# Kernel optimization log

Measured on AMD Instinct MI355X. Metric: run time of the kernel, lower is better.

The kernel has to match this reference:

```python
import jax, jax.numpy as jnp
import numpy as np

# Static dims (from init_kwargs / input_specs)
B, D, H, W, T, C = 1, 16, 32, 32, 4, 128
G, NH = 4, 8
HD = C // NH
NW = (D // G) * (H // G) * (W // G)   # windows per sample
N = G ** 3 * T                         # tokens per window (T-major ordering)
MLP_H = 4 * C
SCALE = 1.0 / float(np.sqrt(HD))
EPS = 1e-5


def _ln(x, g, b):
    m = x.mean(-1, keepdims=True)
    v = ((x - m) ** 2).mean(-1, keepdims=True)
    return (x - m) / jnp.sqrt(v + EPS) * g + b


def setup_inputs() -> dict:
    key = jax.random.key(0)
    ks = jax.random.split(key, 10)
    s = 0.02
    return {
        "x": jax.random.normal(ks[0], (B, D, H, W, T, C), jnp.float32),
        "norm1_g": jnp.ones((C,), jnp.float32),
        "norm1_b": jnp.zeros((C,), jnp.float32),
        "pos_embed": jax.random.normal(ks[1], (G, G, G, C), jnp.float32) * s,
        "time_embed": jax.random.normal(ks[2], (T, 1, 1, 1, C), jnp.float32) * s,
        "qkv_w": jax.random.normal(ks[3], (3 * C, C), jnp.float32) * s,
        "qkv_b": jnp.zeros((3 * C,), jnp.float32),
        "proj_w": jax.random.normal(ks[4], (C, C), jnp.float32) * s,
        "proj_b": jnp.zeros((C,), jnp.float32),
        "conv_w": jax.random.normal(ks[5], (C, 1, 3, 3, 3), jnp.float32) * s,  # depthwise
        "conv_b": jnp.zeros((C,), jnp.float32),
        "exln_g": jnp.ones((C,), jnp.float32),
        "exln_b": jnp.zeros((C,), jnp.float32),
        "norm2_g": jnp.ones((C,), jnp.float32),
        "norm2_b": jnp.zeros((C,), jnp.float32),
        "fc1_w": jax.random.normal(ks[6], (MLP_H, C), jnp.float32) * s,
        "fc1_b": jnp.zeros((MLP_H,), jnp.float32),
        "fc2_w": jax.random.normal(ks[7], (C, MLP_H), jnp.float32) * s,
        "fc2_b": jnp.zeros((C,), jnp.float32),
    }


def reference(x, norm1_g, norm1_b, pos_embed, time_embed, qkv_w, qkv_b,
              proj_w, proj_b, conv_w, conv_b, exln_g, exln_b,
              norm2_g, norm2_b, fc1_w, fc1_b, fc2_w, fc2_b):
    # --- window partition (lsda_flag=0, local SDA; dims divisible by G -> padding=0) ---
    xw = x.reshape(B, D // G, G, H // G, G, W // G, G, T, C)
    xw = xw.transpose(0, 1, 3, 5, 7, 2, 4, 6, 8)   # (B, Dg, Hg, Wg, T, G, G, G, C)
    xw = xw.reshape(B * NW, N, C)                   # token dim is T-major over (T,G,G,G)

    # --- pre-norm + window attention ---
    h = _ln(xw, norm1_g, norm1_b)
    h = h.reshape(B * NW, T, G, G, G, C)
    h = (h + pos_embed + time_embed).reshape(B * NW, N, C)  # learned spatial + temporal PE
    qkv = (h @ qkv_w.T + qkv_b).reshape(B * NW, N, 3, NH, HD).transpose(2, 0, 3, 1, 4)
    q, k, v = qkv[0] * SCALE, qkv[1], qkv[2]        # (B_, NH, N, HD)
    attn = jax.nn.softmax(jnp.einsum('bhnd,bhmd->bhnm', q, k), axis=-1)
    o = jnp.einsum('bhnm,bhmd->bhnd', attn, v).transpose(0, 2, 1, 3).reshape(B * NW, N, C)
    o = o @ proj_w.T + proj_b

    # --- window merge (inverse of partition) ---
    y = o.reshape(B, D // G, H // G, W // G, T, G, G, G, C)
    y = y.transpose(0, 1, 5, 2, 6, 3, 7, 4, 8).reshape(B, D, H, W, T, C)

    # --- depthwise 3x3x3 Conv3d over (D,H,W), T folded into batch, then LN ---
    xc = y.transpose(0, 4, 5, 1, 2, 3).reshape(B * T, C, D, H, W)
    xc = jax.lax.conv_general_dilated(
        xc, conv_w, window_strides=(1, 1, 1),
        padding=((1, 1), (1, 1), (1, 1)),
        feature_group_count=C,
        dimension_numbers=('NCDHW', 'OIDHW', 'NCDHW'))
    xc = xc + conv_b[None, :, None, None, None]
    y = xc.reshape(B, T, C, D, H, W).transpose(0, 3, 4, 5, 1, 2)
    y = _ln(y, exln_g, exln_b)

    # --- MLP with residual: x = mlp(norm2(x)) + x ---
    h2 = _ln(y, norm2_g, norm2_b)
    h2 = jax.nn.gelu(h2 @ fc1_w.T + fc1_b, approximate=False)
    h2 = h2 @ fc2_w.T + fc2_b
    return h2 + y
```

## Files before the change

kernel.cpp:

```cpp
#include <hip/hip_runtime.h>
#include <hip/hip_bf16.h>


typedef __attribute__((ext_vector_type(8))) short  s16x8;
typedef __attribute__((ext_vector_type(4))) short  s16x4;
typedef __attribute__((ext_vector_type(4))) float  f32x4;
typedef __attribute__((ext_vector_type(8))) _Float16 f16x8;
typedef __attribute__((ext_vector_type(4))) _Float16 f16x4;

#define CC    128
#define NWIN  256
#define TOKS  65536
#define SCALE 0.25f
#define LNEPS 1e-5f
#define PD 18
#define PH 34
#define PW 34
#define PSITES (PD*PH*PW)
#define Y1P_SHORTS ((size_t)PSITES*512)

__device__ __forceinline__ float b2f(short s) {
  union { unsigned u; float f; } c; c.u = ((unsigned)(unsigned short)s) << 16; return c.f;
}
__device__ __forceinline__ short f2b(float f) {
  __hip_bfloat16 h = __float2bfloat16(f);
  return *reinterpret_cast<short*>(&h);
}
__device__ __forceinline__ float fast_gelu(float x) {
  float u = 1.595769122f * x * fmaf(0.044715f, x*x, 1.0f);
  return x / (1.0f + __expf(-u));
}

__device__ __forceinline__ f32x4 mfma16x16x16_bf16(s16x4 a, s16x4 b, f32x4 c) {
#if __has_builtin(__builtin_amdgcn_mfma_f32_16x16x16_bf16)
  return __builtin_amdgcn_mfma_f32_16x16x16_bf16(a, b, c, 0, 0, 0);
#elif __has_builtin(__builtin_amdgcn_mfma_f32_16x16x16bf16_1k)
  return __builtin_amdgcn_mfma_f32_16x16x16bf16_1k(a, b, c, 0, 0, 0);
#else
  f32x4 d;
  asm("v_mfma_f32_16x16x16_bf16 %0, %1, %2, %3" : "=v"(d) : "v"(a), "v"(b), "v"(c));
  return d;
#endif
}

__device__ __forceinline__ void gload16(const short* g, short* l) {
  __builtin_amdgcn_global_load_lds(
      (const __attribute__((address_space(1))) void*)g,
      (__attribute__((address_space(3))) void*)l, 16, 0, 0);
}

__global__ void prep_kernel(const float* __restrict__ qkv_w, const float* __restrict__ proj_w,
                            const float* __restrict__ fc1_w, const float* __restrict__ fc2_w,
                            const float* __restrict__ conv_w,
                            __hip_bfloat16* wq, __hip_bfloat16* wp,
                            __hip_bfloat16* w1, __hip_bfloat16* w2, float* cwT) {
  int idx = blockIdx.x * 256 + threadIdx.x;
  if (idx < 49152) {
    wq[idx] = __float2bfloat16(qkv_w[idx]);
  } else if (idx < 65536) {
    wp[idx - 49152] = __float2bfloat16(proj_w[idx - 49152]);
  } else if (idx < 131072) {
    w1[idx - 65536] = __float2bfloat16(fc1_w[idx - 65536]);
  } else if (idx < 196608) {
    w2[idx - 131072] = __float2bfloat16(fc2_w[idx - 131072]);
  } else if (idx < 196608 + 27*128) {
    int j = idx - 196608;
    int tap = j >> 7, c = j & 127;
    cwT[tap*128 + c] = conv_w[c*27 + tap];
  }
}

__global__ __launch_bounds__(256) void border_zero_kernel(short* __restrict__ y1p) {
  int idx = blockIdx.x*256 + threadIdx.x;
  if (idx >= PSITES*64) return;
  int site = idx >> 6;
  int w = site % PW, hh = (site / PW) % PH, d = site / (PW*PH);
  if (d != 0 && d != PD-1 && hh != 0 && hh != PH-1 && w != 0 && w != PW-1) return;
  *(s16x8*)&y1p[(size_t)site*512 + (idx & 63)*8] = (s16x8)0;
}

__global__ __launch_bounds__(256) void ln1_pe_kernel(
    const float* __restrict__ x, const float* __restrict__ g, const float* __restrict__ b,
    const float* __restrict__ pos, const float* __restrict__ te,
    __hip_bfloat16* __restrict__ hb) {
  const int tid = threadIdx.x;
  const int tk = blockIdx.x*8 + (tid >> 5);
  const int c4 = (tid & 31) * 4;
  const int wid = tk >> 8, n = tk & 255;
  const int t = n >> 6, gd = (n >> 4) & 3, gh = (n >> 2) & 3, gw = n & 3;
  const int wd = wid >> 6, wh = (wid >> 3) & 7, ww = wid & 7;
  const int d = wd*4 + gd, h = wh*4 + gh, w = ww*4 + gw;
  const size_t xoff = ((size_t)((d*32 + h)*32 + w)*4 + t) * CC;
  f32x4 v = *(const f32x4*)&x[xoff + c4];
  float s  = (v.x + v.y) + (v.z + v.w);
  float sq = (v.x*v.x + v.y*v.y) + (v.z*v.z + v.w*v.w);
#pragma unroll
  for (int m = 1; m <= 16; m <<= 1) { s += __shfl_xor(s, m); sq += __shfl_xor(sq, m); }
  const float mean = s * (1.f/128.f);
  const float var  = sq * (1.f/128.f) - mean*mean;
  const float rstd = rsqrtf(var + LNEPS);
  const int pb = ((gd*4 + gh)*4 + gw) * CC, tb = t * CC;
  f32x4 gv = *(const f32x4*)&g[c4];
  f32x4 bv = *(const f32x4*)&b[c4];
  f32x4 pv = *(const f32x4*)&pos[pb + c4];
  f32x4 tv = *(const f32x4*)&te[tb + c4];
  s16x4 o;
  o[0] = f2b((v.x - mean)*rstd*gv.x + bv.x + pv.x + tv.x);
  o[1] = f2b((v.y - mean)*rstd*gv.y + bv.y + pv.y + tv.y);
  o[2] = f2b((v.z - mean)*rstd*gv.z + bv.z + pv.z + tv.z);
  o[3] = f2b((v.w - mean)*rstd*gv.w + bv.w + pv.w + tv.w);
  *(s16x4*)&((short*)hb)[(size_t)tk*CC + c4] = o;
}

template <int MODE, int KK>
__global__ __launch_bounds__(256) void gemm_kernel(
    const short* __restrict__ Ag, const short* __restrict__ Wg,
    const float* __restrict__ bias,
    void* __restrict__ out0, const _Float16* __restrict__ resid) {
  __shared__ __align__(16) short As[128*64];
  __shared__ __align__(16) short Bs[128*64];
  const int tid = threadIdx.x;
  const int m0 = blockIdx.x * 128;
  const int n0 = blockIdx.y * 128;
  const int lane = tid & 63, wv = tid >> 6;
  const int wr = wv >> 1, wc = wv & 1;
  const int fr = lane & 15, kg = lane >> 4;

  f32x4 acc[4][4];
#pragma unroll
  for (int i = 0; i < 4; ++i)
#pragma unroll
    for (int j = 0; j < 4; ++j) acc[i][j] = (f32x4)0.f;

#pragma unroll
  for (int kc = 0; kc < KK; kc += 64) {
    __syncthreads();
#pragma unroll
    for (int i = 0; i < 4; ++i) {
      const int e = i*2048 + tid*8;
      const int row = e >> 6, col = e & 63;
      gload16(Ag + (size_t)(m0 + row)*KK + kc + col, &As[i*2048 + wv*512]);
      gload16(Wg + (size_t)(n0 + row)*KK + kc + col, &Bs[i*2048 + wv*512]);
    }
    __syncthreads();
#pragma unroll
    for (int ks = 0; ks < 2; ++ks) {
      s16x8 a[4], b[4];
#pragma unroll
      for (int i = 0; i < 4; ++i)
        a[i] = *(const s16x8*)&As[(wr*64 + i*16 + fr)*64 + ks*32 + kg*8];
#pragma unroll
      for (int j = 0; j < 4; ++j)
        b[j] = *(const s16x8*)&Bs[(wc*64 + j*16 + fr)*64 + ks*32 + kg*8];
#pragma unroll
      for (int i = 0; i < 4; ++i)
#pragma unroll
        for (int j = 0; j < 4; ++j)
          acc[i][j] = __builtin_amdgcn_mfma_f32_16x16x32_bf16(b[j], a[i], acc[i][j], 0, 0, 0);
    }
  }

  const int nbb = n0 + wc*64 + kg*4;
  f32x4 bj4[4];
#pragma unroll
  for (int j = 0; j < 4; ++j) bj4[j] = *(const f32x4*)&bias[nbb + j*16];

#pragma unroll
  for (int i = 0; i < 4; ++i) {
    const int m = m0 + wr*64 + i*16 + fr;
    if constexpr (MODE == 0) {
      short* qs = (short*)out0;
      const int sec = n0 >> 7;
      const float scl = (sec == 0) ? SCALE : 1.0f;
      const int wid = m >> 8, ntok = m & 255;
      const int rowbase = sec*8388608 + (wid*8)*4096 + ntok*16 + (nbb & 15);
#pragma unroll
      for (int j = 0; j < 4; ++j) {
        const int head = ((nbb + j*16) >> 4) & 7;
        f32x4 v = acc[i][j];
        s16x4 o;
        o[0] = f2b(fmaf(v[0], scl, bj4[j].x*scl));
        o[1] = f2b(fmaf(v[1], scl, bj4[j].y*scl));
        o[2] = f2b(fmaf(v[2], scl, bj4[j].z*scl));
        o[3] = f2b(fmaf(v[3], scl, bj4[j].w*scl));
        *(s16x4*)&qs[rowbase + head*4096] = o;
      }
    } else if constexpr (MODE == 1) {
      short* y1o = (short*)out0;
      const int wid = m >> 8, ntok = m & 255;
      const int t = ntok >> 6, gd = (ntok >> 4) & 3, gh = (ntok >> 2) & 3, gw = ntok & 3;
      const int wd = wid >> 6, wh = (wid >> 3) & 7, ww = wid & 7;
      const int sr = (((wd*4 + gd + 1)*PH + wh*4 + gh + 1)*PW + ww*4 + gw + 1)*4 + t;
      const int base = sr*CC + nbb;
#pragma unroll
      for (int j = 0; j < 4; ++j) {
        f32x4 v = acc[i][j];
        s16x4 o;
        o[0] = f2b(v[0] + bj4[j].x); o[1] = f2b(v[1] + bj4[j].y);
        o[2] = f2b(v[2] + bj4[j].z); o[3] = f2b(v[3] + bj4[j].w);
        *(s16x4*)&y1o[base + j*16] = o;
      }
    } else if constexpr (MODE == 2) {
      short* gp = (short*)out0;
      const int base = m*512 + nbb;
#pragma unroll
      for (int j = 0; j < 4; ++j) {
        f32x4 v = acc[i][j];
        s16x4 o;
        o[0] = f2b(fast_gelu(v[0] + bj4[j].x)); o[1] = f2b(fast_gelu(v[1] + bj4[j].y));
        o[2] = f2b(fast_gelu(v[2] + bj4[j].z)); o[3] = f2b(fast_gelu(v[3] + bj4[j].w));
        *(s16x4*)&gp[base + j*16] = o;
      }
    } else {
      float* outp = (float*)out0;
      const int base = m*CC + nbb;
#pragma unroll
      for (int j = 0; j < 4; ++j) {
        f32x4 v = acc[i][j];
        f16x4 rz = *(const f16x4*)&resid[base + j*16];
        f32x4 o;
        o.x = v[0] + bj4[j].x + (float)rz[0]; o.y = v[1] + bj4[j].y + (float)rz[1];
        o.z = v[2] + bj4[j].z + (float)rz[2]; o.w = v[3] + bj4[j].w + (float)rz[3];
        *(f32x4*)&outp[base + j*16] = o;
      }
    }
  }
}

#define KPAD 20
#define VPAD 264
__global__ __launch_bounds__(256) void attn_mfma_kernel(
    const __hip_bfloat16* __restrict__ qb, const __hip_bfloat16* __restrict__ kb,
    const __hip_bfloat16* __restrict__ vb, __hip_bfloat16* __restrict__ ob) {
  __shared__ __align__(16) short kL[256*KPAD];
  __shared__ __align__(16) short vT[16*VPAD];
  const int bh = blockIdx.x;
  const int wid = bh >> 3, head = bh & 7;
  const int tid = threadIdx.x;
  const short* kg = (const short*)kb + (size_t)bh*4096;
  const short* vg = (const short*)vb + (size_t)bh*4096;
  const short* qg = (const short*)qb + (size_t)bh*4096;
  {
    s16x8 a0 = *(const s16x8*)&kg[tid*16];
    s16x8 a1 = *(const s16x8*)&kg[tid*16 + 8];
    *(s16x8*)&kL[tid*KPAD]     = a0;
    *(s16x8*)&kL[tid*KPAD + 8] = a1;
    s16x8 b0 = *(const s16x8*)&vg[tid*16];
    s16x8 b1 = *(const s16x8*)&vg[tid*16 + 8];
#pragma unroll
    for (int d = 0; d < 8; ++d) {
      vT[d*VPAD + tid]     = b0[d];
      vT[(d+8)*VPAD + tid] = b1[d];
    }
  }
  __syncthreads();
  const int wv = tid >> 6, lane = tid & 63;
  const int fr = lane & 15, hi = lane >> 4;
  s16x4 kfrag[16], vfrag[16];
#pragma unroll
  for (int t = 0; t < 16; ++t) {
    kfrag[t] = *(const s16x4*)&kL[(t*16 + fr)*KPAD + hi*4];
    vfrag[t] = *(const s16x4*)&vT[fr*VPAD + t*16 + hi*4];
  }
  short* obs = (short*)ob;
  for (int qt = 0; qt < 4; ++qt) {
    const int q0 = wv*64 + qt*16;
    s16x4 qfrag = *(const s16x4*)&qg[(q0 + fr)*16 + hi*4];
    f32x4 st[16];
#pragma unroll
    for (int kt = 0; kt < 16; ++kt)
      st[kt] = mfma16x16x16_bf16(kfrag[kt], qfrag, (f32x4)0.f);
    float den = 0.f;
    f32x4 oacc = (f32x4)0.f;
#pragma unroll
    for (int kt = 0; kt < 16; ++kt) {
      float e0 = __expf(st[kt][0]), e1 = __expf(st[kt][1]);
      float e2 = __expf(st[kt][2]), e3 = __expf(st[kt][3]);
      den += (e0 + e1) + (e2 + e3);
      s16x4 pa;
      pa[0] = f2b(e0); pa[1] = f2b(e1); pa[2] = f2b(e2); pa[3] = f2b(e3);
      oacc = mfma16x16x16_bf16(vfrag[kt], pa, oacc);
    }
    den += __shfl_xor(den, 16);
    den += __shfl_xor(den, 32);
    float inv = 1.f / den;
    s16x4 ov;
    ov[0] = f2b(oacc[0]*inv); ov[1] = f2b(oacc[1]*inv);
    ov[2] = f2b(oacc[2]*inv); ov[3] = f2b(oacc[3]*inv);
    *(s16x4*)&obs[((size_t)wid*256 + q0 + fr)*CC + head*16 + hi*4] = ov;
  }
}

__global__ __launch_bounds__(256) void conv_ln_kernel(
    const __hip_bfloat16* __restrict__ y1p, const float* __restrict__ wT,
    const float* __restrict__ cb,
    const float* __restrict__ exg, const float* __restrict__ exb,
    const float* __restrict__ n2g, const float* __restrict__ n2b,
    _Float16* __restrict__ yb, __hip_bfloat16* __restrict__ h2) {
  const int tid = threadIdx.x;
  const int sp = blockIdx.x*16 + (tid >> 4);
  const int cbase = (tid & 15) * 8;
  const int w = sp & 31, h = (sp >> 5) & 31, d = sp >> 10;
  const int psite = ((d+1)*PH + (h+1))*PW + (w+1);
  const short* base = (const short*)y1p + (size_t)psite*512 + cbase;

  float acc[4][8];
  {
    f32x4 cb0 = *(const f32x4*)&cb[cbase];
    f32x4 cb1 = *(const f32x4*)&cb[cbase + 4];
#pragma unroll
    for (int t = 0; t < 4; ++t) {
      acc[t][0]=cb0.x; acc[t][1]=cb0.y; acc[t][2]=cb0.z; acc[t][3]=cb0.w;
      acc[t][4]=cb1.x; acc[t][5]=cb1.y; acc[t][6]=cb1.z; acc[t][7]=cb1.w;
    }
  }

#pragma unroll
  for (int dd = -1; dd <= 1; ++dd)
#pragma unroll
    for (int dh = -1; dh <= 1; ++dh)
#pragma unroll
      for (int dw = -1; dw <= 1; ++dw) {
        const int tap = ((dd+1)*3 + (dh+1))*3 + (dw+1);
        const int toff = ((dd*PH + dh)*PW + dw)*512;
        f32x4 w0 = *(const f32x4*)&wT[tap*CC + cbase];
        f32x4 w1 = *(const f32x4*)&wT[tap*CC + cbase + 4];
#pragma unroll
        for (int t = 0; t < 4; ++t) {
          s16x8 v = *(const s16x8*)(base + toff + t*CC);
          acc[t][0] = fmaf(b2f(v[0]), w0.x, acc[t][0]);
          acc[t][1] = fmaf(b2f(v[1]), w0.y, acc[t][1]);
          acc[t][2] = fmaf(b2f(v[2]), w0.z, acc[t][2]);
          acc[t][3] = fmaf(b2f(v[3]), w0.w, acc[t][3]);
          acc[t][4] = fmaf(b2f(v[4]), w1.x, acc[t][4]);
          acc[t][5] = fmaf(b2f(v[5]), w1.y, acc[t][5]);
          acc[t][6] = fmaf(b2f(v[6]), w1.z, acc[t][6]);
          acc[t][7] = fmaf(b2f(v[7]), w1.w, acc[t][7]);
        }
      }

  f32x4 eg0 = *(const f32x4*)&exg[cbase], eg1 = *(const f32x4*)&exg[cbase+4];
  f32x4 eb0 = *(const f32x4*)&exb[cbase], eb1 = *(const f32x4*)&exb[cbase+4];
  f32x4 ng0 = *(const f32x4*)&n2g[cbase], ng1 = *(const f32x4*)&n2g[cbase+4];
  f32x4 nb0 = *(const f32x4*)&n2b[cbase], nb1 = *(const f32x4*)&n2b[cbase+4];
  float eg[8] = {eg0.x,eg0.y,eg0.z,eg0.w,eg1.x,eg1.y,eg1.z,eg1.w};
  float eb[8] = {eb0.x,eb0.y,eb0.z,eb0.w,eb1.x,eb1.y,eb1.z,eb1.w};
  float ng[8] = {ng0.x,ng0.y,ng0.z,ng0.w,ng1.x,ng1.y,ng1.z,ng1.w};
  float nb[8] = {nb0.x,nb0.y,nb0.z,nb0.w,nb1.x,nb1.y,nb1.z,nb1.w};

#pragma unroll
  for (int t = 0; t < 4; ++t) {
    float s = 0.f, sq = 0.f;
#pragma unroll
    for (int c = 0; c < 8; ++c) { s += acc[t][c]; sq = fmaf(acc[t][c], acc[t][c], sq); }
#pragma unroll
    for (int m = 1; m <= 8; m <<= 1) { s += __shfl_xor(s, m); sq += __shfl_xor(sq, m); }
    float mean = s * (1.f/128.f);
    float var  = sq * (1.f/128.f) - mean*mean;
    float rstd = rsqrtf(var + LNEPS);
    float y[8];
    f16x8 yo;
#pragma unroll
    for (int c = 0; c < 8; ++c) {
      y[c] = (acc[t][c] - mean)*rstd*eg[c] + eb[c];
      yo[c] = (_Float16)y[c];
    }
    *(f16x8*)&yb[(size_t)(sp*4 + t)*CC + cbase] = yo;
    float s2 = 0.f, sq2 = 0.f;
#pragma unroll
    for (int c = 0; c < 8; ++c) { s2 += y[c]; sq2 = fmaf(y[c], y[c], sq2); }
#pragma unroll
    for (int m = 1; m <= 8; m <<= 1) { s2 += __shfl_xor(s2, m); sq2 += __shfl_xor(sq2, m); }
    float mean2 = s2 * (1.f/128.f);
    float var2  = sq2 * (1.f/128.f) - mean2*mean2;
    float rstd2 = rsqrtf(var2 + LNEPS);
    s16x8 ho;
#pragma unroll
    for (int c = 0; c < 8; ++c)
      ho[c] = f2b((y[c] - mean2)*rstd2*ng[c] + nb[c]);
    *(s16x8*)&((short*)h2)[(size_t)(sp*4 + t)*CC + cbase] = ho;
  }
}

extern "C" void kernel_launch(void* const* d_in, const int* in_sizes, int n_in,
                              void* d_out, int out_size, void* d_ws, size_t ws_size,
                              hipStream_t stream) {
  const float* x      = (const float*)d_in[0];
  const float* n1g    = (const float*)d_in[1];
  const float* n1b    = (const float*)d_in[2];
  const float* pos    = (const float*)d_in[3];
  const float* te     = (const float*)d_in[4];
  const float* qkv_w  = (const float*)d_in[5];
  const float* qkv_b  = (const float*)d_in[6];
  const float* proj_w = (const float*)d_in[7];
  const float* proj_b = (const float*)d_in[8];
  const float* conv_w = (const float*)d_in[9];
  const float* conv_b = (const float*)d_in[10];
  const float* exg    = (const float*)d_in[11];
  const float* exb    = (const float*)d_in[12];
  const float* n2g    = (const float*)d_in[13];
  const float* n2b    = (const float*)d_in[14];
  const float* fc1_w  = (const float*)d_in[15];
  const float* fc1_b  = (const float*)d_in[16];
  const float* fc2_w  = (const float*)d_in[17];
  const float* fc2_b  = (const float*)d_in[18];

  char* wsb = (char*)d_ws;
  __hip_bfloat16* wq  = (__hip_bfloat16*)(wsb);
  __hip_bfloat16* wp  = (__hip_bfloat16*)(wsb + 98304);
  __hip_bfloat16* w1  = (__hip_bfloat16*)(wsb + 131072);
  __hip_bfloat16* w2  = (__hip_bfloat16*)(wsb + 262144);
  float*          cwT = (float*)(wsb + 393216);

  const size_t A_OFF = (size_t)1 << 20;
  const size_t B_OFF = A_OFF + ((size_t)16 << 20);
  const size_t C_OFF = B_OFF + ((size_t)48 << 20);

  __hip_bfloat16* hbuf = (__hip_bfloat16*)(wsb + A_OFF);
  __hip_bfloat16* obuf = (__hip_bfloat16*)(wsb + A_OFF);
  __hip_bfloat16* h2in = (__hip_bfloat16*)(wsb + A_OFF);
  __hip_bfloat16* qkvb = (__hip_bfloat16*)(wsb + B_OFF);
  __hip_bfloat16* qb   = qkvb;
  __hip_bfloat16* kb   = qkvb + 8388608;
  __hip_bfloat16* vb   = qkvb + 16777216;
  __hip_bfloat16* y1p  = (__hip_bfloat16*)(wsb + B_OFF);
  _Float16* yb = (_Float16*)(wsb + B_OFF + ((size_t)24 << 20));
  __hip_bfloat16* gbuf = (__hip_bfloat16*)(wsb + C_OFF);

  prep_kernel<<<782, 256, 0, stream>>>(qkv_w, proj_w, fc1_w, fc2_w, conv_w,
                                       wq, wp, w1, w2, cwT);
  ln1_pe_kernel<<<TOKS/8, 256, 0, stream>>>(x, n1g, n1b, pos, te, hbuf);
  gemm_kernel<0, 128><<<dim3(TOKS/128, 3), 256, 0, stream>>>(
      (const short*)hbuf, (const short*)wq, qkv_b, (void*)qkvb, nullptr);
  attn_mfma_kernel<<<NWIN*8, 256, 0, stream>>>(qb, kb, vb, obuf);
  border_zero_kernel<<<(PSITES*64 + 255)/256, 256, 0, stream>>>((short*)y1p);
  gemm_kernel<1, 128><<<dim3(TOKS/128, 1), 256, 0, stream>>>(
      (const short*)obuf, (const short*)wp, proj_b, (void*)y1p, nullptr);
  conv_ln_kernel<<<16384/16, 256, 0, stream>>>(y1p, cwT, conv_b,
      exg, exb, n2g, n2b, yb, h2in);
  gemm_kernel<2, 128><<<dim3(TOKS/128, 4), 256, 0, stream>>>(
      (const short*)h2in, (const short*)w1, fc1_b, (void*)gbuf, nullptr);
  gemm_kernel<3, 512><<<dim3(TOKS/128, 1), 256, 0, stream>>>(
      (const short*)gbuf, (const short*)w2, fc2_b, (void*)d_out, yb);
}
```

Measured before the change: 171.3 us.

## Fuse prep and LN1 launches, double-buffer fc2 GEMM, split conv work per thread

Merges the weight-conversion and LN1+embedding kernels into one launch to save a kernel launch. Adds a double-buffered LDS path to the GEMM, used only for the K=512 fc2 GEMM, so the next K tile loads while MFMAs run on the current one. The depthwise conv+LN kernel now gives each thread two time steps instead of four, doubling the grid to raise occupancy and parallelism. The double-buffered path doubles LDS use for that GEMM, which may lower occupancy.

```diff
diff --git a/kernel.cpp b/kernel.cpp
--- a/kernel.cpp
+++ b/kernel.cpp
@@ -18,6 +18,7 @@
 #define PW 34
 #define PSITES (PD*PH*PW)
 #define Y1P_SHORTS ((size_t)PSITES*512)
+#define PREP_BLOCKS 782
 
 __device__ __forceinline__ float b2f(short s) {
   union { unsigned u; float f; } c; c.u = ((unsigned)(unsigned short)s) << 16; return c.f;
@@ -49,42 +50,34 @@
       (__attribute__((address_space(3))) void*)l, 16, 0, 0);
 }
 
-__global__ void prep_kernel(const float* __restrict__ qkv_w, const float* __restrict__ proj_w,
-                            const float* __restrict__ fc1_w, const float* __restrict__ fc2_w,
-                            const float* __restrict__ conv_w,
-                            __hip_bfloat16* wq, __hip_bfloat16* wp,
-                            __hip_bfloat16* w1, __hip_bfloat16* w2, float* cwT) {
-  int idx = blockIdx.x * 256 + threadIdx.x;
-  if (idx < 49152) {
-    wq[idx] = __float2bfloat16(qkv_w[idx]);
-  } else if (idx < 65536) {
-    wp[idx - 49152] = __float2bfloat16(proj_w[idx - 49152]);
-  } else if (idx < 131072) {
-    w1[idx - 65536] = __float2bfloat16(fc1_w[idx - 65536]);
-  } else if (idx < 196608) {
-    w2[idx - 131072] = __float2bfloat16(fc2_w[idx - 131072]);
-  } else if (idx < 196608 + 27*128) {
-    int j = idx - 196608;
-    int tap = j >> 7, c = j & 127;
-    cwT[tap*128 + c] = conv_w[c*27 + tap];
-  }
-}
-
-__global__ __launch_bounds__(256) void border_zero_kernel(short* __restrict__ y1p) {
-  int idx = blockIdx.x*256 + threadIdx.x;
-  if (idx >= PSITES*64) return;
-  int site = idx >> 6;
-  int w = site % PW, hh = (site / PW) % PH, d = site / (PW*PH);
-  if (d != 0 && d != PD-1 && hh != 0 && hh != PH-1 && w != 0 && w != PW-1) return;
-  *(s16x8*)&y1p[(size_t)site*512 + (idx & 63)*8] = (s16x8)0;
-}
-
-__global__ __launch_bounds__(256) void ln1_pe_kernel(
-    const float* __restrict__ x, const float* __restrict__ g, const float* __restrict__ b,
-    const float* __restrict__ pos, const float* __restrict__ te,
-    __hip_bfloat16* __restrict__ hb) {
+__global__ __launch_bounds__(256) void setup_kernel(
+    const float* __restrict__ qkv_w, const float* __restrict__ proj_w,
+    const float* __restrict__ fc1_w, const float* __restrict__ fc2_w,
+    const float* __restrict__ conv_w,
+    __hip_bfloat16* wq, __hip_bfloat16* wp,
+    __hip_bfloat16* w1, __hip_bfloat16* w2, float* cwT,
+    const float* __restrict__ x, const float* __restrict__ g,
+    const float* __restrict__ b, const float* __restrict__ pos,
+    const float* __restrict__ te, __hip_bfloat16* __restrict__ hb) {
+  if (blockIdx.x < PREP_BLOCKS) {
+    int idx = blockIdx.x * 256 + threadIdx.x;
+    if (idx < 49152) {
+      wq[idx] = __float2bfloat16(qkv_w[idx]);
+    } else if (idx < 65536) {
+      wp[idx - 49152] = __float2bfloat16(proj_w[idx - 49152]);
+    } else if (idx < 131072) {
+      w1[idx - 65536] = __float2bfloat16(fc1_w[idx - 65536]);
+    } else if (idx < 196608) {
+      w2[idx - 131072] = __float2bfloat16(fc2_w[idx - 131072]);
+    } else if (idx < 196608 + 27*128) {
+      int j = idx - 196608;
+      int tap = j >> 7, c = j & 127;
+      cwT[tap*128 + c] = conv_w[c*27 + tap];
+    }
+    return;
+  }
   const int tid = threadIdx.x;
-  const int tk = blockIdx.x*8 + (tid >> 5);
+  const int tk = (blockIdx.x - PREP_BLOCKS)*8 + (tid >> 5);
   const int c4 = (tid & 31) * 4;
   const int wid = tk >> 8, n = tk & 255;
   const int t = n >> 6, gd = (n >> 4) & 3, gh = (n >> 2) & 3, gw = n & 3;
@@ -112,13 +105,22 @@
   *(s16x4*)&((short*)hb)[(size_t)tk*CC + c4] = o;
 }
 
-template <int MODE, int KK>
+__global__ __launch_bounds__(256) void border_zero_kernel(short* __restrict__ y1p) {
+  int idx = blockIdx.x*256 + threadIdx.x;
+  if (idx >= PSITES*64) return;
+  int site = idx >> 6;
+  int w = site % PW, hh = (site / PW) % PH, d = site / (PW*PH);
+  if (d != 0 && d != PD-1 && hh != 0 && hh != PH-1 && w != 0 && w != PW-1) return;
+  *(s16x8*)&y1p[(size_t)site*512 + (idx & 63)*8] = (s16x8)0;
+}
+
+template <int MODE, int KK, int DB>
 __global__ __launch_bounds__(256) void gemm_kernel(
     const short* __restrict__ Ag, const short* __restrict__ Wg,
     const float* __restrict__ bias,
     void* __restrict__ out0, const _Float16* __restrict__ resid) {
-  __shared__ __align__(16) short As[128*64];
-  __shared__ __align__(16) short Bs[128*64];
+  __shared__ __align__(16) short As[DB + 1][128*64];
+  __shared__ __align__(16) short Bs[DB + 1][128*64];
   const int tid = threadIdx.x;
   const int m0 = blockIdx.x * 128;
   const int n0 = blockIdx.y * 128;
@@ -132,31 +134,73 @@
 #pragma unroll
     for (int j = 0; j < 4; ++j) acc[i][j] = (f32x4)0.f;
 
-#pragma unroll
-  for (int kc = 0; kc < KK; kc += 64) {
-    __syncthreads();
+  if constexpr (DB == 0) {
+#pragma unroll
+    for (int kc = 0; kc < KK; kc += 64) {
+      __syncthreads();
+#pragma unroll
+      for (int i = 0; i < 4; ++i) {
+        const int e = i*2048 + tid*8;
+        const int row = e >> 6, col = e & 63;
+        gload16(Ag + (size_t)(m0 + row)*KK + kc + col, &As[0][i*2048 + wv*512]);
+        gload16(Wg + (size_t)(n0 + row)*KK + kc + col, &Bs[0][i*2048 + wv*512]);
+      }
+      __syncthreads();
+#pragma unroll
+      for (int ks = 0; ks < 2; ++ks) {
+        s16x8 a[4], b[4];
+#pragma unroll
+        for (int i = 0; i < 4; ++i)
+          a[i] = *(const s16x8*)&As[0][(wr*64 + i*16 + fr)*64 + ks*32 + kg*8];
+#pragma unroll
+        for (int j = 0; j < 4; ++j)
+          b[j] = *(const s16x8*)&Bs[0][(wc*64 + j*16 + fr)*64 + ks*32 + kg*8];
+#pragma unroll
+        for (int i = 0; i < 4; ++i)
+#pragma unroll
+          for (int j = 0; j < 4; ++j)
+            acc[i][j] = __builtin_amdgcn_mfma_f32_16x16x32_bf16(b[j], a[i], acc[i][j], 0, 0, 0);
+      }
+    }
+  } else {
+    constexpr int NT = KK / 64;
 #pragma unroll
     for (int i = 0; i < 4; ++i) {
       const int e = i*2048 + tid*8;
       const int row = e >> 6, col = e & 63;
-      gload16(Ag + (size_t)(m0 + row)*KK + kc + col, &As[i*2048 + wv*512]);
-      gload16(Wg + (size_t)(n0 + row)*KK + kc + col, &Bs[i*2048 + wv*512]);
+      gload16(Ag + (size_t)(m0 + row)*KK + col, &As[0][i*2048 + wv*512]);
+      gload16(Wg + (size_t)(n0 + row)*KK + col, &Bs[0][i*2048 + wv*512]);
     }
     __syncthreads();
 #pragma unroll
-    for (int ks = 0; ks < 2; ++ks) {
-      s16x8 a[4], b[4];
-#pragma unroll
-      for (int i = 0; i < 4; ++i)
-        a[i] = *(const s16x8*)&As[(wr*64 + i*16 + fr)*64 + ks*32 + kg*8];
-#pragma unroll
-      for (int j = 0; j < 4; ++j)
-        b[j] = *(const s16x8*)&Bs[(wc*64 + j*16 + fr)*64 + ks*32 + kg*8];
-#pragma unroll
-      for (int i = 0; i < 4; ++i)
+    for (int t = 0; t < NT; ++t) {
+      const int cur = t & 1;
+      if (t + 1 < NT) {
+        const int kc = (t + 1) * 64;
+#pragma unroll
+        for (int i = 0; i < 4; ++i) {
+          const int e = i*2048 + tid*8;
+          const int row = e >> 6, col = e & 63;
+          gload16(Ag + (size_t)(m0 + row)*KK + kc + col, &As[cur^1][i*2048 + wv*512]);
+          gload16(Wg + (size_t)(n0 + row)*KK + kc + col, &Bs[cur^1][i*2048 + wv*512]);
+        }
+      }
+#pragma unroll
+      for (int ks = 0; ks < 2; ++ks) {
+        s16x8 a[4], b[4];
+#pragma unroll
+        for (int i = 0; i < 4; ++i)
+          a[i] = *(const s16x8*)&As[cur][(wr*64 + i*16 + fr)*64 + ks*32 + kg*8];
 #pragma unroll
         for (int j = 0; j < 4; ++j)
-          acc[i][j] = __builtin_amdgcn_mfma_f32_16x16x32_bf16(b[j], a[i], acc[i][j], 0, 0, 0);
+          b[j] = *(const s16x8*)&Bs[cur][(wc*64 + j*16 + fr)*64 + ks*32 + kg*8];
+#pragma unroll
+        for (int i = 0; i < 4; ++i)
+#pragma unroll
+          for (int j = 0; j < 4; ++j)
+            acc[i][j] = __builtin_amdgcn_mfma_f32_16x16x32_bf16(b[j], a[i], acc[i][j], 0, 0, 0);
+      }
+      __syncthreads();
     }
   }
 
@@ -298,18 +342,19 @@
     const float* __restrict__ n2g, const float* __restrict__ n2b,
     _Float16* __restrict__ yb, __hip_bfloat16* __restrict__ h2) {
   const int tid = threadIdx.x;
-  const int sp = blockIdx.x*16 + (tid >> 4);
+  const int sp = blockIdx.x*8 + (tid >> 5);
+  const int tp = (tid >> 4) & 1;
   const int cbase = (tid & 15) * 8;
   const int w = sp & 31, h = (sp >> 5) & 31, d = sp >> 10;
   const int psite = ((d+1)*PH + (h+1))*PW + (w+1);
-  const short* base = (const short*)y1p + (size_t)psite*512 + cbase;
-
-  float acc[4][8];
+  const short* base = (const short*)y1p + (size_t)psite*512 + tp*2*CC + cbase;
+
+  float acc[2][8];
   {
     f32x4 cb0 = *(const f32x4*)&cb[cbase];
     f32x4 cb1 = *(const f32x4*)&cb[cbase + 4];
 #pragma unroll
-    for (int t = 0; t < 4; ++t) {
+    for (int t = 0; t < 2; ++t) {
       acc[t][0]=cb0.x; acc[t][1]=cb0.y; acc[t][2]=cb0.z; acc[t][3]=cb0.w;
       acc[t][4]=cb1.x; acc[t][5]=cb1.y; acc[t][6]=cb1.z; acc[t][7]=cb1.w;
     }
@@ -326,7 +371,7 @@
         f32x4 w0 = *(const f32x4*)&wT[tap*CC + cbase];
         f32x4 w1 = *(const f32x4*)&wT[tap*CC + cbase + 4];
 #pragma unroll
-        for (int t = 0; t < 4; ++t) {
+        for (int t = 0; t < 2; ++t) {
           s16x8 v = *(const s16x8*)(base + toff + t*CC);
           acc[t][0] = fmaf(b2f(v[0]), w0.x, acc[t][0]);
           acc[t][1] = fmaf(b2f(v[1]), w0.y, acc[t][1]);
@@ -349,7 +394,7 @@
   float nb[8] = {nb0.x,nb0.y,nb0.z,nb0.w,nb1.x,nb1.y,nb1.z,nb1.w};
 
 #pragma unroll
-  for (int t = 0; t < 4; ++t) {
+  for (int t = 0; t < 2; ++t) {
     float s = 0.f, sq = 0.f;
 #pragma unroll
     for (int c = 0; c < 8; ++c) { s += acc[t][c]; sq = fmaf(acc[t][c], acc[t][c], sq); }
@@ -365,7 +410,8 @@
       y[c] = (acc[t][c] - mean)*rstd*eg[c] + eb[c];
       yo[c] = (_Float16)y[c];
     }
-    *(f16x8*)&yb[(size_t)(sp*4 + t)*CC + cbase] = yo;
+    const int tok = sp*4 + tp*2 + t;
+    *(f16x8*)&yb[(size_t)tok*CC + cbase] = yo;
     float s2 = 0.f, sq2 = 0.f;
 #pragma unroll
     for (int c = 0; c < 8; ++c) { s2 += y[c]; sq2 = fmaf(y[c], y[c], sq2); }
@@ -378,7 +424,7 @@
 #pragma unroll
     for (int c = 0; c < 8; ++c)
       ho[c] = f2b((y[c] - mean2)*rstd2*ng[c] + nb[c]);
-    *(s16x8*)&((short*)h2)[(size_t)(sp*4 + t)*CC + cbase] = ho;
+    *(s16x8*)&((short*)h2)[(size_t)tok*CC + cbase] = ho;
   }
 }
 
@@ -427,19 +473,19 @@
   _Float16* yb = (_Float16*)(wsb + B_OFF + ((size_t)24 << 20));
   __hip_bfloat16* gbuf = (__hip_bfloat16*)(wsb + C_OFF);
 
-  prep_kernel<<<782, 256, 0, stream>>>(qkv_w, proj_w, fc1_w, fc2_w, conv_w,
-                                       wq, wp, w1, w2, cwT);
-  ln1_pe_kernel<<<TOKS/8, 256, 0, stream>>>(x, n1g, n1b, pos, te, hbuf);
-  gemm_kernel<0, 128><<<dim3(TOKS/128, 3), 256, 0, stream>>>(
+  setup_kernel<<<PREP_BLOCKS + TOKS/8, 256, 0, stream>>>(
+      qkv_w, proj_w, fc1_w, fc2_w, conv_w, wq, wp, w1, w2, cwT,
+      x, n1g, n1b, pos, te, hbuf);
+  gemm_kernel<0, 128, 0><<<dim3(TOKS/128, 3), 256, 0, stream>>>(
       (const short*)hbuf, (const short*)wq, qkv_b, (void*)qkvb, nullptr);
   attn_mfma_kernel<<<NWIN*8, 256, 0, stream>>>(qb, kb, vb, obuf);
   border_zero_kernel<<<(PSITES*64 + 255)/256, 256, 0, stream>>>((short*)y1p);
-  gemm_kernel<1, 128><<<dim3(TOKS/128, 1), 256, 0, stream>>>(
+  gemm_kernel<1, 128, 0><<<dim3(TOKS/128, 1), 256, 0, stream>>>(
       (const short*)obuf, (const short*)wp, proj_b, (void*)y1p, nullptr);
-  conv_ln_kernel<<<16384/16, 256, 0, stream>>>(y1p, cwT, conv_b,
+  conv_ln_kernel<<<16384/8, 256, 0, stream>>>(y1p, cwT, conv_b,
       exg, exb, n2g, n2b, yb, h2in);
-  gemm_kernel<2, 128><<<dim3(TOKS/128, 4), 256, 0, stream>>>(
+  gemm_kernel<2, 128, 0><<<dim3(TOKS/128, 4), 256, 0, stream>>>(
       (const short*)h2in, (const short*)w1, fc1_b, (void*)gbuf, nullptr);
-  gemm_kernel<3, 512><<<dim3(TOKS/128, 1), 256, 0, stream>>>(
+  gemm_kernel<3, 512, 1><<<dim3(TOKS/128, 1), 256, 0, stream>>>(
       (const short*)gbuf, (const short*)w2, fc2_b, (void*)d_out, yb);
 }
```

After: 169.3 us. Within noise of the previous version (-1.1%).
